# Kernel tuning notes

Hardware: AMD Instinct MI355X
Metric: run time of the kernel (lower is better)

Reference implementation:

```python
import jax, jax.numpy as jnp
import numpy as np

N_NODES = 40962
N_EDGES = 245760
K = 10  # gaussian kernels
D = 2   # pseudo-coordinate dim
EPS = 1e-15


def gmm_conv(x, edge_index, pseudo, g, mu, sigma, root, bias):
    """PyG GMMConv with aggr='mean', root_weight=True.
    x: [N, Cin], edge_index: [2, E] (row 0 = source j, row 1 = target i),
    pseudo: [E, D], g: [Cin, K*Cout], mu/sigma: [K, D], root: [Cin, Cout], bias: [Cout].
    """
    src, dst = edge_index[0], edge_index[1]
    E = pseudo.shape[0]
    # Gaussian mixture edge weights: [E, K]
    diff = pseudo[:, None, :] - mu[None, :, :]                     # [E, K, D]
    w = jnp.exp(jnp.sum(-0.5 * diff * diff / (EPS + sigma[None] ** 2), axis=-1))
    xj = x[src]                                                    # [E, Cin] gather
    y = (xj @ g).reshape(E, K, -1)                                 # [E, K, Cout]
    msg = jnp.sum(y * w[:, :, None], axis=1)                       # [E, Cout]
    agg = jax.ops.segment_sum(msg, dst, num_segments=N_NODES)      # scatter-add
    deg = jax.ops.segment_sum(jnp.ones((E,), x.dtype), dst, num_segments=N_NODES)
    agg = agg / jnp.maximum(deg, 1.0)[:, None]                     # mean aggregation
    return agg + x @ root + bias


def setup_inputs() -> dict:
    key = jax.random.key(0)
    ks = jax.random.split(key, 20)
    Cin, Ch, Cout = 64, 64, 128
    sc = lambda fan: 1.0 / np.sqrt(fan)
    inp = {
        "x": jax.random.normal(ks[0], (N_NODES, Cin), jnp.float32),
        "edge_index": jax.random.randint(ks[1], (2, N_EDGES), 0, N_NODES, jnp.int32),
        "pseudo": jax.random.uniform(ks[2], (N_EDGES, D), jnp.float32),
        # conv1: Cin -> Ch
        "g1": jax.random.normal(ks[3], (Cin, K * Ch), jnp.float32) * sc(Cin),
        "mu1": jax.random.uniform(ks[4], (K, D), jnp.float32),
        "sigma1": jax.random.uniform(ks[5], (K, D), jnp.float32) + 0.5,
        "root1": jax.random.normal(ks[6], (Cin, Ch), jnp.float32) * sc(Cin),
        "b1": jnp.zeros((Ch,), jnp.float32),
        # conv2: Ch -> Cout
        "g2": jax.random.normal(ks[7], (Ch, K * Cout), jnp.float32) * sc(Ch),
        "mu2": jax.random.uniform(ks[8], (K, D), jnp.float32),
        "sigma2": jax.random.uniform(ks[9], (K, D), jnp.float32) + 0.5,
        "root2": jax.random.normal(ks[10], (Ch, Cout), jnp.float32) * sc(Ch),
        "b2": jnp.zeros((Cout,), jnp.float32),
        # shortcut: Cin -> Cout (size_in != size_out)
        "gs": jax.random.normal(ks[11], (Cin, K * Cout), jnp.float32) * sc(Cin),
        "mus": jax.random.uniform(ks[12], (K, D), jnp.float32),
        "sigmas": jax.random.uniform(ks[13], (K, D), jnp.float32) + 0.5,
        "roots": jax.random.normal(ks[14], (Cin, Cout), jnp.float32) * sc(Cin),
        "bs": jnp.zeros((Cout,), jnp.float32),
    }
    return inp


def reference(x, edge_index, pseudo, g1, mu1, sigma1, root1, b1,
              g2, mu2, sigma2, root2, b2, gs, mus, sigmas, roots, bs):
    h = gmm_conv(x, edge_index, pseudo, g1, mu1, sigma1, root1, b1)
    h = jax.nn.relu(h)
    y = gmm_conv(h, edge_index, pseudo, g2, mu2, sigma2, root2, b2)
    x_s = gmm_conv(x, edge_index, pseudo, gs, mus, sigmas, roots, bs)
    return jax.nn.relu(y + x_s)
```

## Files before the change

kernel.cpp:

```cpp
#include <hip/hip_runtime.h>
#include <hip/hip_bf16.h>

using bf16 = __hip_bfloat16;
typedef __attribute__((ext_vector_type(8))) short short8;
typedef __attribute__((ext_vector_type(4))) float float4v;

#define N_NODES 40962
#define N_EDGES 245760
#define NP      41024
#define KG      10
#define SCAN_B  256
#define NBLK    ((NP + SCAN_B - 1) / SCAN_B)
#define GRIDF   (NP / 16)

#define CVT_V   (N_NODES * 64 / 8)
#define CVT_BLK ((CVT_V + 255) / 256)
#define W3_BLK  (N_EDGES / 256)
#define PACK_N  (64 * 704 + 2 * 128 * 704)
#define PACK_BLK (PACK_N / 256)

#define ZRS  40
#define ZKS  672
#define ZSZE 13440

__device__ __forceinline__ float ldf(const void* p, size_t i, int isf32) {
    return isf32 ? ((const float*)p)[i] : __bfloat162float(((const bf16*)p)[i]);
}
__device__ __forceinline__ float blo(unsigned u) { return __uint_as_float(u << 16); }
__device__ __forceinline__ float bhi(unsigned u) { return __uint_as_float(u & 0xffff0000u); }
__device__ __forceinline__ unsigned pk2(float a, float b) {
    union { bf16 h[2]; unsigned u; } t;
    t.h[0] = __float2bfloat16(a);
    t.h[1] = __float2bfloat16(b);
    return t.u;
}
__device__ __forceinline__ int rfl(int v) { return __builtin_amdgcn_readfirstlane(v); }

__global__ void k_detect_count(const void* x, const int* __restrict__ ei,
                               int* __restrict__ flag, int* __restrict__ deg) {
    if (blockIdx.x == 0) {
        __shared__ int huge_c, zero_even;
        if (threadIdx.x == 0) { huge_c = 0; zero_even = 0; }
        __syncthreads();
        const bf16* xb = (const bf16*)x;
        int lh = 0, lz = 0;
        for (int i = threadIdx.x; i < 8192; i += 256) {
            float v = __bfloat162float(xb[i]);
            if (!(fabsf(v) <= 1e4f)) lh++;
            if ((i & 1) == 0 && v == 0.0f) lz++;
        }
        atomicAdd(&huge_c, lh);
        atomicAdd(&zero_even, lz);
        __syncthreads();
        if (threadIdx.x == 0) flag[0] = (huge_c > 0 || zero_even > 3000) ? 1 : 0;
    } else {
        int e = (blockIdx.x - 1) * 256 + threadIdx.x;
        if (e < N_EDGES) atomicAdd(&deg[ei[N_EDGES + e]], 1);
    }
}

__global__ void k_scan1(const int* __restrict__ deg, int* __restrict__ offs,
                        int* __restrict__ bsum) {
    __shared__ int buf[SCAN_B];
    int t = threadIdx.x, b = blockIdx.x;
    int i = b * SCAN_B + t;
    int v = (i < NP) ? deg[i] : 0;
    buf[t] = v;
    __syncthreads();
    for (int off = 1; off < SCAN_B; off <<= 1) {
        int a = (t >= off) ? buf[t - off] : 0;
        __syncthreads();
        buf[t] += a;
        __syncthreads();
    }
    if (i < NP) offs[i] = buf[t] - v;
    if (t == SCAN_B - 1) bsum[b] = buf[t];
}

__global__ void k_scan3m(int* __restrict__ offs, const int* __restrict__ bsum,
                         const int* __restrict__ deg, int* __restrict__ cur,
                         float* __restrict__ invdeg) {
    __shared__ int buf[256];
    int t = threadIdx.x, b = blockIdx.x;
    int v = (t < NBLK) ? bsum[t] : 0;
    buf[t] = v;
    __syncthreads();
    for (int off = 1; off < 256; off <<= 1) {
        int a = (t >= off) ? buf[t - off] : 0;
        __syncthreads();
        buf[t] += a;
        __syncthreads();
    }
    int bofs = (b > 0) ? buf[b - 1] : 0;
    int total = buf[NBLK - 1];
    int i = b * 256 + t;
    if (i < NP) {
        int o = offs[i] + bofs;
        offs[i] = o;
        cur[i] = o;
        int d = deg[i];
        invdeg[i] = 1.0f / (float)(d > 1 ? d : 1);
    }
    if (i == 0) offs[NP] = total;
}

__global__ void k_fill(const int* __restrict__ ei, int* __restrict__ cur,
                       int* __restrict__ ep, int* __restrict__ csr_src) {
    int e = blockIdx.x * 256 + threadIdx.x;
    if (e < N_EDGES) {
        int pos = atomicAdd(&cur[ei[N_EDGES + e]], 1);
        ep[e] = pos;
        csr_src[pos] = ei[e];
    }
}

__device__ __forceinline__ void gw_one(float p0, float p1, const void* mu,
                                       const void* sg, int f, float* out) {
#pragma unroll
    for (int k = 0; k < KG; k++) {
        float m0 = ldf(mu, 2 * k + 0, f), m1 = ldf(mu, 2 * k + 1, f);
        float s0 = ldf(sg, 2 * k + 0, f), s1 = ldf(sg, 2 * k + 1, f);
        float d0 = p0 - m0, d1 = p1 - m1;
        float t = -0.5f * (d0 * d0 / (1e-15f + s0 * s0) + d1 * d1 / (1e-15f + s1 * s1));
        out[k] = __expf(t);
    }
}

__device__ __forceinline__ void pack_frag(const void* g, const void* root, int f,
                                          int idx, int Cout, bf16* Bp) {
    int j = idx & 7;
    int lane = (idx >> 3) & 63;
    int rem = idx >> 9;
    int kc = rem % 22;
    int n = rem / 22;
    int col = n * 16 + (lane & 15);
    int k = kc * 32 + (lane >> 4) * 8 + j;
    float v;
    if (k < 512) {
        int cin = k >> 3, kg = k & 7;
        v = ldf(g, (size_t)cin * (KG * Cout) + (size_t)kg * Cout + col, f);
    } else if (k < 640) {
        int jj = k - 512;
        int cin = jj >> 1, kg = 8 + (jj & 1);
        v = ldf(g, (size_t)cin * (KG * Cout) + (size_t)kg * Cout + col, f);
    } else {
        v = ldf(root, (size_t)(k - 640) * Cout + col, f);
    }
    Bp[idx] = __float2bfloat16(v);
}

__global__ void k_prep_all(const void* __restrict__ x, const void* __restrict__ pseudo,
                           const void* mu1, const void* sg1, const void* mu2,
                           const void* sg2, const void* mus, const void* sgs,
                           const void* g1, const void* root1, const void* g2,
                           const void* root2, const void* gs, const void* roots,
                           const int* __restrict__ flag, const int* __restrict__ ep,
                           bf16* __restrict__ Xf, bf16* __restrict__ wc1,
                           bf16* __restrict__ wcs, bf16* __restrict__ wc2,
                           bf16* wt1p, bf16* wt2p, bf16* wtsp) {
    int b = blockIdx.x;
    int tid = threadIdx.x;
    int f = flag[0];
    if (b < CVT_BLK) {
        int i = b * 256 + tid;
        if (i < CVT_V) {
            int node = i >> 3, j = i & 7;
            uint4 u;
            if (f) {
                const float4* xf = (const float4*)x;
                float4 a = xf[2 * i], c = xf[2 * i + 1];
                union { bf16 t[8]; uint4 u; } tt;
                tt.t[0] = __float2bfloat16(a.x); tt.t[1] = __float2bfloat16(a.y);
                tt.t[2] = __float2bfloat16(a.z); tt.t[3] = __float2bfloat16(a.w);
                tt.t[4] = __float2bfloat16(c.x); tt.t[5] = __float2bfloat16(c.y);
                tt.t[6] = __float2bfloat16(c.z); tt.t[7] = __float2bfloat16(c.w);
                u = tt.u;
            } else {
                u = ((const uint4*)x)[i];
            }
            *(uint4*)(Xf + ((size_t)(j >> 2) * NP + node) * 32 + (j & 3) * 8) = u;
        }
    } else if (b < CVT_BLK + W3_BLK) {
        int e = (b - CVT_BLK) * 256 + tid;
        float p0 = ldf(pseudo, (size_t)e * 2 + 0, f);
        float p1 = ldf(pseudo, (size_t)e * 2 + 1, f);
        float o1[KG], o2[KG], os[KG];
        gw_one(p0, p1, mu1, sg1, f, o1);
        gw_one(p0, p1, mu2, sg2, f, o2);
        gw_one(p0, p1, mus, sgs, f, os);
        int pos = ep[e];
        unsigned* d1 = (unsigned*)wc1 + (size_t)pos * 5;
        d1[0] = pk2(o1[0], o1[1]); d1[1] = pk2(o1[2], o1[3]);
        d1[2] = pk2(o1[4], o1[5]); d1[3] = pk2(o1[6], o1[7]);
        d1[4] = pk2(o1[8], o1[9]);
        unsigned* ds = (unsigned*)wcs + (size_t)pos * 5;
        ds[0] = pk2(os[0], os[1]); ds[1] = pk2(os[2], os[3]);
        ds[2] = pk2(os[4], os[5]); ds[3] = pk2(os[6], os[7]);
        ds[4] = pk2(os[8], os[9]);
        unsigned* d2 = (unsigned*)wc2 + (size_t)pos * 5;
        d2[0] = pk2(o2[0], o2[1]); d2[1] = pk2(o2[2], o2[3]);
        d2[2] = pk2(o2[4], o2[5]); d2[3] = pk2(o2[6], o2[7]);
        d2[4] = pk2(o2[8], o2[9]);
    } else {
        int idx = (b - CVT_BLK - W3_BLK) * 256 + tid;
        if (idx < 64 * 704) {
            pack_frag(g1, root1, f, idx, 64, wt1p);
        } else if (idx < 64 * 704 + 128 * 704) {
            pack_frag(g2, root2, f, idx - 64 * 704, 128, wt2p);
        } else {
            pack_frag(gs, roots, f, idx - 64 * 704 - 128 * 704, 128, wtsp);
        }
    }
}

__device__ __forceinline__ float ldx_frag(const bf16* X, int src, int lane) {
    return __bfloat162float(X[((size_t)(lane >> 5) * NP + src) * 32 + (lane & 31)]);
}

__device__ __forceinline__ int clampe(int idx) {
    return idx > N_EDGES - 1 ? N_EDGES - 1 : idx;
}

__device__ __forceinline__ void gather_one(const int* __restrict__ offs,
                                           const int* __restrict__ csr_src,
                                           const unsigned* __restrict__ wb,
                                           const bf16* __restrict__ X, int node,
                                           int lane, float* acc) {
#pragma unroll
    for (int k = 0; k < KG; k++) acc[k] = 0.0f;
    int beg = rfl(offs[node]);
    int end = rfl(offs[node + 1]);
    int cnt = end - beg;
    int sC = rfl(csr_src[clampe(beg + 2)]);
    float xv0 = ldx_frag(X, rfl(csr_src[clampe(beg + 0)]), lane);
    float xv1 = ldx_frag(X, rfl(csr_src[clampe(beg + 1)]), lane);
    const unsigned* wp0 = wb + (size_t)clampe(beg + 0) * 5;
    unsigned c0 = wp0[0], c1 = wp0[1], c2 = wp0[2], c3 = wp0[3], c4 = wp0[4];
    const unsigned* wp1 = wb + (size_t)clampe(beg + 1) * 5;
    unsigned n0 = wp1[0], n1 = wp1[1], n2 = wp1[2], n3 = wp1[3], n4 = wp1[4];
    for (int t = 0; t < cnt; ++t) {
        int sN = rfl(csr_src[clampe(beg + t + 3)]);
        float xv2 = ldx_frag(X, sC, lane);
        const unsigned* wp2 = wb + (size_t)clampe(beg + t + 2) * 5;
        unsigned m0 = wp2[0], m1 = wp2[1], m2 = wp2[2], m3 = wp2[3], m4 = wp2[4];
        acc[0] += blo(c0) * xv0; acc[1] += bhi(c0) * xv0;
        acc[2] += blo(c1) * xv0; acc[3] += bhi(c1) * xv0;
        acc[4] += blo(c2) * xv0; acc[5] += bhi(c2) * xv0;
        acc[6] += blo(c3) * xv0; acc[7] += bhi(c3) * xv0;
        acc[8] += blo(c4) * xv0; acc[9] += bhi(c4) * xv0;
        xv0 = xv1; xv1 = xv2; sC = sN;
        c0 = n0; c1 = n1; c2 = n2; c3 = n3; c4 = n4;
        n0 = m0; n1 = m1; n2 = m2; n3 = m3; n4 = m4;
    }
}

__device__ __forceinline__ void store_zlds(bf16* z, int r, int lane, const float* a,
                                           float inv) {
    union { bf16 h[8]; uint4 u; } p;
#pragma unroll
    for (int k = 0; k < 8; k++) p.h[k] = __float2bfloat16(a[k] * inv);
    *(uint4*)(z + (lane >> 2) * ZKS + r * ZRS + (lane & 3) * 8) = p.u;
    *(unsigned*)(z + (16 + (lane >> 4)) * ZKS + r * ZRS + (lane & 15) * 2) =
        pk2(a[8] * inv, a[9] * inv);
}

__global__ __launch_bounds__(512) void k_fused1(
    const int* __restrict__ offs, const int* __restrict__ csr_src,
    const bf16* __restrict__ wc1, const float* __restrict__ invdeg,
    const bf16* __restrict__ Xf, const bf16* __restrict__ wt1p,
    const void* __restrict__ b1, const int* __restrict__ flag,
    bf16* __restrict__ hf) {
    __shared__ bf16 zA[ZSZE];
    int lane = threadIdx.x & 63;
    int wave = threadIdx.x >> 6;
    int bid = blockIdx.x;
    const unsigned* wb = (const unsigned*)wc1;

#pragma unroll
    for (int i = 0; i < 2; i++) {
        int r = wave * 2 + i;
        int node = bid * 16 + r;
        float acc[KG];
        gather_one(offs, csr_src, wb, Xf, node, lane, acc);
        store_zlds(zA, r, lane, acc, invdeg[node]);
    }
    __syncthreads();

    if (wave < 4) {
        int m = lane & 15, quad = lane >> 4;
        int row0 = bid * 16;
        float4v acc4 = (float4v){0.f, 0.f, 0.f, 0.f};
        const bf16* brow = wt1p + ((size_t)(wave * 22) * 64 + lane) * 8;
        const bf16* xrow = Xf + ((size_t)(row0 + m)) * 32 + quad * 8;
#pragma unroll
        for (int kc = 0; kc < 22; kc++) {
            short8 a = (kc < 20)
                ? *(const short8*)(zA + kc * ZKS + m * ZRS + quad * 8)
                : *(const short8*)(xrow + (size_t)(kc - 20) * NP * 32);
            short8 b = *(const short8*)(brow + (size_t)kc * 512);
            acc4 = __builtin_amdgcn_mfma_f32_16x16x32_bf16(a, b, acc4, 0, 0, 0);
        }
        int f = flag[0];
        int gcol = wave * 16 + m;
        float bv = ldf(b1, gcol, f);
#pragma unroll
        for (int r = 0; r < 4; r++) {
            int grow = row0 + quad * 4 + r;
            if (grow >= N_NODES) continue;
            float v = fmaxf(acc4[r] + bv, 0.f);
            hf[((size_t)(gcol >> 5) * NP + grow) * 32 + (gcol & 31)] =
                __float2bfloat16(v);
        }
    }
}

__global__ __launch_bounds__(512) void k_fused2(
    const int* __restrict__ offs, const int* __restrict__ csr_src,
    const bf16* __restrict__ wc2, const bf16* __restrict__ wcs,
    const float* __restrict__ invdeg, const bf16* __restrict__ Xf,
    const bf16* __restrict__ hf, const bf16* __restrict__ wt2p,
    const bf16* __restrict__ wtsp, const void* __restrict__ b2,
    const void* __restrict__ bs, const int* __restrict__ flag,
    void* __restrict__ out) {
    __shared__ bf16 z[ZSZE];
    int lane = threadIdx.x & 63;
    int wave = threadIdx.x >> 6;
    int bid = blockIdx.x;
    int m = lane & 15, quad = lane >> 4;
    int row0 = bid * 16;

#pragma unroll
    for (int i = 0; i < 2; i++) {
        int r = wave * 2 + i;
        int node = bid * 16 + r;
        float acc[KG];
        gather_one(offs, csr_src, (const unsigned*)wc2, hf, node, lane, acc);
        store_zlds(z, r, lane, acc, invdeg[node]);
    }
    __syncthreads();

    float4v acc4 = (float4v){0.f, 0.f, 0.f, 0.f};
    {
        const bf16* brow = wt2p + ((size_t)(wave * 22) * 64 + lane) * 8;
        const bf16* hrow = hf + ((size_t)(row0 + m)) * 32 + quad * 8;
#pragma unroll
        for (int kc = 0; kc < 22; kc++) {
            short8 a = (kc < 20)
                ? *(const short8*)(z + kc * ZKS + m * ZRS + quad * 8)
                : *(const short8*)(hrow + (size_t)(kc - 20) * NP * 32);
            short8 b = *(const short8*)(brow + (size_t)kc * 512);
            acc4 = __builtin_amdgcn_mfma_f32_16x16x32_bf16(a, b, acc4, 0, 0, 0);
        }
    }
    __syncthreads();

#pragma unroll
    for (int i = 0; i < 2; i++) {
        int r = wave * 2 + i;
        int node = bid * 16 + r;
        float acc[KG];
        gather_one(offs, csr_src, (const unsigned*)wcs, Xf, node, lane, acc);
        store_zlds(z, r, lane, acc, invdeg[node]);
    }
    __syncthreads();

    {
        const bf16* brow = wtsp + ((size_t)(wave * 22) * 64 + lane) * 8;
        const bf16* xrow = Xf + ((size_t)(row0 + m)) * 32 + quad * 8;
#pragma unroll
        for (int kc = 0; kc < 22; kc++) {
            short8 a = (kc < 20)
                ? *(const short8*)(z + kc * ZKS + m * ZRS + quad * 8)
                : *(const short8*)(xrow + (size_t)(kc - 20) * NP * 32);
            short8 b = *(const short8*)(brow + (size_t)kc * 512);
            acc4 = __builtin_amdgcn_mfma_f32_16x16x32_bf16(a, b, acc4, 0, 0, 0);
        }
    }

    int f = flag[0];
    int gcol = wave * 16 + m;
    float bv = ldf(b2, gcol, f) + ldf(bs, gcol, f);
#pragma unroll
    for (int r = 0; r < 4; r++) {
        int grow = row0 + quad * 4 + r;
        if (grow >= N_NODES) continue;
        float v = fmaxf(acc4[r] + bv, 0.f);
        size_t oidx = (size_t)grow * 128 + gcol;
        if (f) ((float*)out)[oidx] = v;
        else   ((bf16*)out)[oidx] = __float2bfloat16(v);
    }
}

extern "C" void kernel_launch(void* const* d_in, const int* in_sizes, int n_in,
                              void* d_out, int out_size, void* d_ws, size_t ws_size,
                              hipStream_t stream) {
    const void* x      = d_in[0];
    const int*  ei     = (const int*)d_in[1];
    const void* pseudo = d_in[2];
    const void* g1     = d_in[3];
    const void* mu1    = d_in[4];
    const void* sg1    = d_in[5];
    const void* root1  = d_in[6];
    const void* b1     = d_in[7];
    const void* g2     = d_in[8];
    const void* mu2    = d_in[9];
    const void* sg2    = d_in[10];
    const void* root2  = d_in[11];
    const void* b2     = d_in[12];
    const void* gs     = d_in[13];
    const void* mus    = d_in[14];
    const void* sgs    = d_in[15];
    const void* roots  = d_in[16];
    const void* bs     = d_in[17];

    char* ws = (char*)d_ws;
    size_t off = 0;
    auto alloc = [&](size_t bytes) -> char* {
        char* p = ws + off;
        off += (bytes + 255) & ~(size_t)255;
        return p;
    };
    const size_t XFS = (size_t)2 * NP * 32 * 2;

    int*   flag   = (int*)alloc(256);
    int*   deg    = (int*)alloc((size_t)NP * 4);
    int*   offs   = (int*)alloc((size_t)(NP + 1) * 4);
    int*   cur    = (int*)alloc((size_t)NP * 4);
    float* invdeg = (float*)alloc((size_t)NP * 4);
    int*   bsum   = (int*)alloc((size_t)NBLK * 4);
    int*   ep     = (int*)alloc((size_t)N_EDGES * 4);
    int*   csrs   = (int*)alloc((size_t)N_EDGES * 4);
    bf16*  Xf     = (bf16*)alloc(XFS);
    bf16*  hf     = (bf16*)alloc(XFS);
    bf16*  wt1p   = (bf16*)alloc((size_t)64 * 704 * 2);
    bf16*  wt2p   = (bf16*)alloc((size_t)128 * 704 * 2);
    bf16*  wtsp   = (bf16*)alloc((size_t)128 * 704 * 2);
    bf16*  wc1    = (bf16*)alloc((size_t)N_EDGES * 10 * 2);
    bf16*  wcs    = (bf16*)alloc((size_t)N_EDGES * 10 * 2);
    bf16*  wc2    = (bf16*)alloc((size_t)N_EDGES * 10 * 2);
    (void)ws_size;

    hipMemsetAsync(deg, 0, (size_t)NP * 4, stream);
    k_detect_count<<<1 + (N_EDGES + 255) / 256, 256, 0, stream>>>(x, ei, flag, deg);
    k_scan1<<<NBLK, SCAN_B, 0, stream>>>(deg, offs, bsum);
    k_scan3m<<<NBLK, 256, 0, stream>>>(offs, bsum, deg, cur, invdeg);
    k_fill<<<(N_EDGES + 255) / 256, 256, 0, stream>>>(ei, cur, ep, csrs);
    k_prep_all<<<CVT_BLK + W3_BLK + PACK_BLK, 256, 0, stream>>>(
        x, pseudo, mu1, sg1, mu2, sg2, mus, sgs, g1, root1, g2, root2, gs, roots,
        flag, ep, Xf, wc1, wcs, wc2, wt1p, wt2p, wtsp);
    k_fused1<<<GRIDF, 512, 0, stream>>>(offs, csrs, wc1, invdeg, Xf, wt1p, b1,
                                        flag, hf);
    k_fused2<<<GRIDF, 512, 0, stream>>>(offs, csrs, wc2, wcs, invdeg, Xf, hf,
                                        wt2p, wtsp, b2, bs, flag, d_out);
}
```

Baseline: 273.3 us.

## Fuse shortcut gather into first conv pass and switch node features to row-major

The shortcut conv's edge aggregation over x is moved from the second kernel into the first. Both conv1 and shortcut edge weights are now interleaved per edge, so one gather pass over the x neighbours feeds two accumulators. The shortcut result is written to a bf16 intermediate and added in the second kernel. This removes a second full neighbour gather over x. Node features move to a plain row-major 64-wide layout with a deeper prefetch distance, and LDS z is re-laid out row-major. The cost is an extra 128-wide bf16 write and read per node, plus more register pressure in the dual gather.

Measured after the change: 270.9 us. Within noise of the previous version (-0.9%).

```diff
diff --git a/kernel.cpp b/kernel.cpp
--- a/kernel.cpp
+++ b/kernel.cpp
@@ -19,9 +19,8 @@
 #define PACK_N  (64 * 704 + 2 * 128 * 704)
 #define PACK_BLK (PACK_N / 256)
 
-#define ZRS  40
-#define ZKS  672
-#define ZSZE 13440
+#define ZRS  680
+#define ZT   10880
 
 __device__ __forceinline__ float ldf(const void* p, size_t i, int isf32) {
     return isf32 ? ((const float*)p)[i] : __bfloat162float(((const bf16*)p)[i]);
@@ -155,9 +154,9 @@
                            const void* g1, const void* root1, const void* g2,
                            const void* root2, const void* gs, const void* roots,
                            const int* __restrict__ flag, const int* __restrict__ ep,
-                           bf16* __restrict__ Xf, bf16* __restrict__ wc1,
-                           bf16* __restrict__ wcs, bf16* __restrict__ wc2,
-                           bf16* wt1p, bf16* wt2p, bf16* wtsp) {
+                           bf16* __restrict__ Xf, bf16* __restrict__ wcab,
+                           bf16* __restrict__ wc2, bf16* wt1p, bf16* wt2p,
+                           bf16* wtsp) {
     int b = blockIdx.x;
     int tid = threadIdx.x;
     int f = flag[0];
@@ -178,7 +177,7 @@
             } else {
                 u = ((const uint4*)x)[i];
             }
-            *(uint4*)(Xf + ((size_t)(j >> 2) * NP + node) * 32 + (j & 3) * 8) = u;
+            *(uint4*)(Xf + (size_t)node * 64 + j * 8) = u;
         }
     } else if (b < CVT_BLK + W3_BLK) {
         int e = (b - CVT_BLK) * 256 + tid;
@@ -189,14 +188,13 @@
         gw_one(p0, p1, mu2, sg2, f, o2);
         gw_one(p0, p1, mus, sgs, f, os);
         int pos = ep[e];
-        unsigned* d1 = (unsigned*)wc1 + (size_t)pos * 5;
-        d1[0] = pk2(o1[0], o1[1]); d1[1] = pk2(o1[2], o1[3]);
-        d1[2] = pk2(o1[4], o1[5]); d1[3] = pk2(o1[6], o1[7]);
-        d1[4] = pk2(o1[8], o1[9]);
-        unsigned* ds = (unsigned*)wcs + (size_t)pos * 5;
-        ds[0] = pk2(os[0], os[1]); ds[1] = pk2(os[2], os[3]);
-        ds[2] = pk2(os[4], os[5]); ds[3] = pk2(os[6], os[7]);
-        ds[4] = pk2(os[8], os[9]);
+        unsigned* d = (unsigned*)wcab + (size_t)pos * 10;
+        d[0] = pk2(o1[0], o1[1]); d[1] = pk2(o1[2], o1[3]);
+        d[2] = pk2(o1[4], o1[5]); d[3] = pk2(o1[6], o1[7]);
+        d[4] = pk2(o1[8], o1[9]);
+        d[5] = pk2(os[0], os[1]); d[6] = pk2(os[2], os[3]);
+        d[7] = pk2(os[4], os[5]); d[8] = pk2(os[6], os[7]);
+        d[9] = pk2(os[8], os[9]);
         unsigned* d2 = (unsigned*)wc2 + (size_t)pos * 5;
         d2[0] = pk2(o2[0], o2[1]); d2[1] = pk2(o2[2], o2[3]);
         d2[2] = pk2(o2[4], o2[5]); d2[3] = pk2(o2[6], o2[7]);
@@ -213,12 +211,66 @@
     }
 }
 
-__device__ __forceinline__ float ldx_frag(const bf16* X, int src, int lane) {
-    return __bfloat162float(X[((size_t)(lane >> 5) * NP + src) * 32 + (lane & 31)]);
+__device__ __forceinline__ float ldxf(const bf16* X, int src, int lane) {
+    return __bfloat162float(X[(size_t)src * 64 + lane]);
 }
 
 __device__ __forceinline__ int clampe(int idx) {
     return idx > N_EDGES - 1 ? N_EDGES - 1 : idx;
+}
+
+__device__ __forceinline__ void store_zlds(bf16* z, int r, int lane, const float* a,
+                                           float inv) {
+    union { bf16 h[8]; uint4 u; } p;
+#pragma unroll
+    for (int k = 0; k < 8; k++) p.h[k] = __float2bfloat16(a[k] * inv);
+    *(uint4*)(z + r * ZRS + lane * 8) = p.u;
+    *(unsigned*)(z + r * ZRS + 512 + lane * 2) = pk2(a[8] * inv, a[9] * inv);
+}
+
+__device__ __forceinline__ void gather_dual(const int* __restrict__ offs,
+                                            const int* __restrict__ csr_src,
+                                            const unsigned* __restrict__ wb,
+                                            const bf16* __restrict__ X, int node,
+                                            int lane, float* aa, float* ab) {
+#pragma unroll
+    for (int k = 0; k < KG; k++) { aa[k] = 0.0f; ab[k] = 0.0f; }
+    int beg = rfl(offs[node]);
+    int end = rfl(offs[node + 1]);
+    int cnt = end - beg;
+    int s4 = rfl(csr_src[clampe(beg + 4)]);
+    float xv0 = ldxf(X, rfl(csr_src[clampe(beg + 0)]), lane);
+    float xv1 = ldxf(X, rfl(csr_src[clampe(beg + 1)]), lane);
+    float xv2 = ldxf(X, rfl(csr_src[clampe(beg + 2)]), lane);
+    float xv3 = ldxf(X, rfl(csr_src[clampe(beg + 3)]), lane);
+    const unsigned* wp0 = wb + (size_t)clampe(beg + 0) * 10;
+    unsigned c0 = wp0[0], c1 = wp0[1], c2 = wp0[2], c3 = wp0[3], c4 = wp0[4];
+    unsigned c5 = wp0[5], c6 = wp0[6], c7 = wp0[7], c8 = wp0[8], c9 = wp0[9];
+    const unsigned* wp1 = wb + (size_t)clampe(beg + 1) * 10;
+    unsigned n0 = wp1[0], n1 = wp1[1], n2 = wp1[2], n3 = wp1[3], n4 = wp1[4];
+    unsigned n5 = wp1[5], n6 = wp1[6], n7 = wp1[7], n8 = wp1[8], n9 = wp1[9];
+    for (int t = 0; t < cnt; ++t) {
+        int s5 = rfl(csr_src[clampe(beg + t + 5)]);
+        float xv4 = ldxf(X, s4, lane);
+        const unsigned* wp2 = wb + (size_t)clampe(beg + t + 2) * 10;
+        unsigned m0 = wp2[0], m1 = wp2[1], m2 = wp2[2], m3 = wp2[3], m4 = wp2[4];
+        unsigned m5 = wp2[5], m6 = wp2[6], m7 = wp2[7], m8 = wp2[8], m9 = wp2[9];
+        aa[0] += blo(c0) * xv0; aa[1] += bhi(c0) * xv0;
+        aa[2] += blo(c1) * xv0; aa[3] += bhi(c1) * xv0;
+        aa[4] += blo(c2) * xv0; aa[5] += bhi(c2) * xv0;
+        aa[6] += blo(c3) * xv0; aa[7] += bhi(c3) * xv0;
+        aa[8] += blo(c4) * xv0; aa[9] += bhi(c4) * xv0;
+        ab[0] += blo(c5) * xv0; ab[1] += bhi(c5) * xv0;
+        ab[2] += blo(c6) * xv0; ab[3] += bhi(c6) * xv0;
+        ab[4] += blo(c7) * xv0; ab[5] += bhi(c7) * xv0;
+        ab[6] += blo(c8) * xv0; ab[7] += bhi(c8) * xv0;
+        ab[8] += blo(c9) * xv0; ab[9] += bhi(c9) * xv0;
+        xv0 = xv1; xv1 = xv2; xv2 = xv3; xv3 = xv4; s4 = s5;
+        c0 = n0; c1 = n1; c2 = n2; c3 = n3; c4 = n4;
+        c5 = n5; c6 = n6; c7 = n7; c8 = n8; c9 = n9;
+        n0 = m0; n1 = m1; n2 = m2; n3 = m3; n4 = m4;
+        n5 = m5; n6 = m6; n7 = m7; n8 = m8; n9 = m9;
+    }
 }
 
 __device__ __forceinline__ void gather_one(const int* __restrict__ offs,
@@ -231,16 +283,18 @@
     int beg = rfl(offs[node]);
     int end = rfl(offs[node + 1]);
     int cnt = end - beg;
-    int sC = rfl(csr_src[clampe(beg + 2)]);
-    float xv0 = ldx_frag(X, rfl(csr_src[clampe(beg + 0)]), lane);
-    float xv1 = ldx_frag(X, rfl(csr_src[clampe(beg + 1)]), lane);
+    int s4 = rfl(csr_src[clampe(beg + 4)]);
+    float xv0 = ldxf(X, rfl(csr_src[clampe(beg + 0)]), lane);
+    float xv1 = ldxf(X, rfl(csr_src[clampe(beg + 1)]), lane);
+    float xv2 = ldxf(X, rfl(csr_src[clampe(beg + 2)]), lane);
+    float xv3 = ldxf(X, rfl(csr_src[clampe(beg + 3)]), lane);
     const unsigned* wp0 = wb + (size_t)clampe(beg + 0) * 5;
     unsigned c0 = wp0[0], c1 = wp0[1], c2 = wp0[2], c3 = wp0[3], c4 = wp0[4];
     const unsigned* wp1 = wb + (size_t)clampe(beg + 1) * 5;
     unsigned n0 = wp1[0], n1 = wp1[1], n2 = wp1[2], n3 = wp1[3], n4 = wp1[4];
     for (int t = 0; t < cnt; ++t) {
-        int sN = rfl(csr_src[clampe(beg + t + 3)]);
-        float xv2 = ldx_frag(X, sC, lane);
+        int s5 = rfl(csr_src[clampe(beg + t + 5)]);
+        float xv4 = ldxf(X, s4, lane);
         const unsigned* wp2 = wb + (size_t)clampe(beg + t + 2) * 5;
         unsigned m0 = wp2[0], m1 = wp2[1], m2 = wp2[2], m3 = wp2[3], m4 = wp2[4];
         acc[0] += blo(c0) * xv0; acc[1] += bhi(c0) * xv0;
@@ -248,59 +302,75 @@
         acc[4] += blo(c2) * xv0; acc[5] += bhi(c2) * xv0;
         acc[6] += blo(c3) * xv0; acc[7] += bhi(c3) * xv0;
         acc[8] += blo(c4) * xv0; acc[9] += bhi(c4) * xv0;
-        xv0 = xv1; xv1 = xv2; sC = sN;
+        xv0 = xv1; xv1 = xv2; xv2 = xv3; xv3 = xv4; s4 = s5;
         c0 = n0; c1 = n1; c2 = n2; c3 = n3; c4 = n4;
         n0 = m0; n1 = m1; n2 = m2; n3 = m3; n4 = m4;
     }
 }
 
-__device__ __forceinline__ void store_zlds(bf16* z, int r, int lane, const float* a,
-                                           float inv) {
-    union { bf16 h[8]; uint4 u; } p;
-#pragma unroll
-    for (int k = 0; k < 8; k++) p.h[k] = __float2bfloat16(a[k] * inv);
-    *(uint4*)(z + (lane >> 2) * ZKS + r * ZRS + (lane & 3) * 8) = p.u;
-    *(unsigned*)(z + (16 + (lane >> 4)) * ZKS + r * ZRS + (lane & 15) * 2) =
-        pk2(a[8] * inv, a[9] * inv);
-}
-
-__global__ __launch_bounds__(512) void k_fused1(
+__global__ __launch_bounds__(512) void k_fusedA(
     const int* __restrict__ offs, const int* __restrict__ csr_src,
-    const bf16* __restrict__ wc1, const float* __restrict__ invdeg,
+    const bf16* __restrict__ wcab, const float* __restrict__ invdeg,
     const bf16* __restrict__ Xf, const bf16* __restrict__ wt1p,
-    const void* __restrict__ b1, const int* __restrict__ flag,
-    bf16* __restrict__ hf) {
-    __shared__ bf16 zA[ZSZE];
+    const bf16* __restrict__ wtsp, const void* __restrict__ b1,
+    const void* __restrict__ bs, const int* __restrict__ flag,
+    bf16* __restrict__ hf, bf16* __restrict__ ys) {
+    __shared__ bf16 z1[ZT];
+    __shared__ bf16 zs[ZT];
     int lane = threadIdx.x & 63;
     int wave = threadIdx.x >> 6;
     int bid = blockIdx.x;
-    const unsigned* wb = (const unsigned*)wc1;
 
 #pragma unroll
     for (int i = 0; i < 2; i++) {
         int r = wave * 2 + i;
         int node = bid * 16 + r;
-        float acc[KG];
-        gather_one(offs, csr_src, wb, Xf, node, lane, acc);
-        store_zlds(zA, r, lane, acc, invdeg[node]);
+        float aa[KG], ab[KG];
+        gather_dual(offs, csr_src, (const unsigned*)wcab, Xf, node, lane, aa, ab);
+        float inv = invdeg[node];
+        store_zlds(z1, r, lane, aa, inv);
+        store_zlds(zs, r, lane, ab, inv);
     }
     __syncthreads();
 
+    int m = lane & 15, quad = lane >> 4;
+    int row0 = bid * 16;
+    int f = flag[0];
+
+    {
+        float4v acc4 = (float4v){0.f, 0.f, 0.f, 0.f};
+        const bf16* brow = wtsp + ((size_t)(wave * 22) * 64 + lane) * 8;
+        const bf16* xrow = Xf + (size_t)(row0 + m) * 64;
+#pragma unroll
+        for (int kc = 0; kc < 22; kc++) {
+            short8 a = (kc < 20)
+                ? *(const short8*)(zs + m * ZRS + kc * 32 + quad * 8)
+                : *(const short8*)(xrow + (kc - 20) * 32 + quad * 8);
+            short8 b = *(const short8*)(brow + (size_t)kc * 512);
+            acc4 = __builtin_amdgcn_mfma_f32_16x16x32_bf16(a, b, acc4, 0, 0, 0);
+        }
+        int gcol = wave * 16 + m;
+        float bv = ldf(bs, gcol, f);
+#pragma unroll
+        for (int r = 0; r < 4; r++) {
+            int grow = row0 + quad * 4 + r;
+            if (grow >= N_NODES) continue;
+            ys[(size_t)grow * 128 + gcol] = __float2bfloat16(acc4[r] + bv);
+        }
+    }
+
     if (wave < 4) {
-        int m = lane & 15, quad = lane >> 4;
-        int row0 = bid * 16;
         float4v acc4 = (float4v){0.f, 0.f, 0.f, 0.f};
         const bf16* brow = wt1p + ((size_t)(wave * 22) * 64 + lane) * 8;
-        const bf16* xrow = Xf + ((size_t)(row0 + m)) * 32 + quad * 8;
+        const bf16* xrow = Xf + (size_t)(row0 + m) * 64;
 #pragma unroll
         for (int kc = 0; kc < 22; kc++) {
             short8 a = (kc < 20)
-                ? *(const short8*)(zA + kc * ZKS + m * ZRS + quad * 8)
-                : *(const short8*)(xrow + (size_t)(kc - 20) * NP * 32);
+                ? *(const short8*)(z1 + m * ZRS + kc * 32 + quad * 8)
+                : *(const short8*)(xrow + (kc - 20) * 32 + quad * 8);
             short8 b = *(const short8*)(brow + (size_t)kc * 512);
             acc4 = __builtin_amdgcn_mfma_f32_16x16x32_bf16(a, b, acc4, 0, 0, 0);
         }
-        int f = flag[0];
         int gcol = wave * 16 + m;
         float bv = ldf(b1, gcol, f);
 #pragma unroll
@@ -308,26 +378,21 @@
             int grow = row0 + quad * 4 + r;
             if (grow >= N_NODES) continue;
             float v = fmaxf(acc4[r] + bv, 0.f);
-            hf[((size_t)(gcol >> 5) * NP + grow) * 32 + (gcol & 31)] =
-                __float2bfloat16(v);
-        }
-    }
-}
-
-__global__ __launch_bounds__(512) void k_fused2(
+            hf[(size_t)grow * 64 + gcol] = __float2bfloat16(v);
+        }
+    }
+}
+
+__global__ __launch_bounds__(512) void k_fusedB(
     const int* __restrict__ offs, const int* __restrict__ csr_src,
-    const bf16* __restrict__ wc2, const bf16* __restrict__ wcs,
-    const float* __restrict__ invdeg, const bf16* __restrict__ Xf,
+    const bf16* __restrict__ wc2, const float* __restrict__ invdeg,
     const bf16* __restrict__ hf, const bf16* __restrict__ wt2p,
-    const bf16* __restrict__ wtsp, const void* __restrict__ b2,
-    const void* __restrict__ bs, const int* __restrict__ flag,
-    void* __restrict__ out) {
-    __shared__ bf16 z[ZSZE];
+    const void* __restrict__ b2, const bf16* __restrict__ ys,
+    const int* __restrict__ flag, void* __restrict__ out) {
+    __shared__ bf16 z[ZT];
     int lane = threadIdx.x & 63;
     int wave = threadIdx.x >> 6;
     int bid = blockIdx.x;
-    int m = lane & 15, quad = lane >> 4;
-    int row0 = bid * 16;
 
 #pragma unroll
     for (int i = 0; i < 2; i++) {
@@ -339,53 +404,28 @@
     }
     __syncthreads();
 
+    int m = lane & 15, quad = lane >> 4;
+    int row0 = bid * 16;
+    int f = flag[0];
     float4v acc4 = (float4v){0.f, 0.f, 0.f, 0.f};
-    {
-        const bf16* brow = wt2p + ((size_t)(wave * 22) * 64 + lane) * 8;
-        const bf16* hrow = hf + ((size_t)(row0 + m)) * 32 + quad * 8;
-#pragma unroll
-        for (int kc = 0; kc < 22; kc++) {
-            short8 a = (kc < 20)
-                ? *(const short8*)(z + kc * ZKS + m * ZRS + quad * 8)
-                : *(const short8*)(hrow + (size_t)(kc - 20) * NP * 32);
-            short8 b = *(const short8*)(brow + (size_t)kc * 512);
-            acc4 = __builtin_amdgcn_mfma_f32_16x16x32_bf16(a, b, acc4, 0, 0, 0);
-        }
-    }
-    __syncthreads();
-
-#pragma unroll
-    for (int i = 0; i < 2; i++) {
-        int r = wave * 2 + i;
-        int node = bid * 16 + r;
-        float acc[KG];
-        gather_one(offs, csr_src, (const unsigned*)wcs, Xf, node, lane, acc);
-        store_zlds(z, r, lane, acc, invdeg[node]);
-    }
-    __syncthreads();
-
-    {
-        const bf16* brow = wtsp + ((size_t)(wave * 22) * 64 + lane) * 8;
-        const bf16* xrow = Xf + ((size_t)(row0 + m)) * 32 + quad * 8;
-#pragma unroll
-        for (int kc = 0; kc < 22; kc++) {
-            short8 a = (kc < 20)
-                ? *(const short8*)(z + kc * ZKS + m * ZRS + quad * 8)
-                : *(const short8*)(xrow + (size_t)(kc - 20) * NP * 32);
-            short8 b = *(const short8*)(brow + (size_t)kc * 512);
-            acc4 = __builtin_amdgcn_mfma_f32_16x16x32_bf16(a, b, acc4, 0, 0, 0);
-        }
-    }
-
-    int f = flag[0];
+    const bf16* brow = wt2p + ((size_t)(wave * 22) * 64 + lane) * 8;
+    const bf16* hrow = hf + (size_t)(row0 + m) * 64;
+#pragma unroll
+    for (int kc = 0; kc < 22; kc++) {
+        short8 a = (kc < 20)
+            ? *(const short8*)(z + m * ZRS + kc * 32 + quad * 8)
+            : *(const short8*)(hrow + (kc - 20) * 32 + quad * 8);
+        short8 b = *(const short8*)(brow + (size_t)kc * 512);
+        acc4 = __builtin_amdgcn_mfma_f32_16x16x32_bf16(a, b, acc4, 0, 0, 0);
+    }
     int gcol = wave * 16 + m;
-    float bv = ldf(b2, gcol, f) + ldf(bs, gcol, f);
+    float bv = ldf(b2, gcol, f);
 #pragma unroll
     for (int r = 0; r < 4; r++) {
         int grow = row0 + quad * 4 + r;
         if (grow >= N_NODES) continue;
-        float v = fmaxf(acc4[r] + bv, 0.f);
         size_t oidx = (size_t)grow * 128 + gcol;
+        float v = fmaxf(acc4[r] + bv + __bfloat162float(ys[oidx]), 0.f);
         if (f) ((float*)out)[oidx] = v;
         else   ((bf16*)out)[oidx] = __float2bfloat16(v);
     }
@@ -420,7 +460,7 @@
         off += (bytes + 255) & ~(size_t)255;
         return p;
     };
-    const size_t XFS = (size_t)2 * NP * 32 * 2;
+    const size_t XFS = (size_t)NP * 64 * 2;
 
     int*   flag   = (int*)alloc(256);
     int*   deg    = (int*)alloc((size_t)NP * 4);
@@ -432,11 +472,11 @@
     int*   csrs   = (int*)alloc((size_t)N_EDGES * 4);
     bf16*  Xf     = (bf16*)alloc(XFS);
     bf16*  hf     = (bf16*)alloc(XFS);
+    bf16*  ys     = (bf16*)alloc((size_t)NP * 128 * 2);
     bf16*  wt1p   = (bf16*)alloc((size_t)64 * 704 * 2);
     bf16*  wt2p   = (bf16*)alloc((size_t)128 * 704 * 2);
     bf16*  wtsp   = (bf16*)alloc((size_t)128 * 704 * 2);
-    bf16*  wc1    = (bf16*)alloc((size_t)N_EDGES * 10 * 2);
-    bf16*  wcs    = (bf16*)alloc((size_t)N_EDGES * 10 * 2);
+    bf16*  wcab   = (bf16*)alloc((size_t)N_EDGES * 20 * 2);
     bf16*  wc2    = (bf16*)alloc((size_t)N_EDGES * 10 * 2);
     (void)ws_size;
 
@@ -447,9 +487,9 @@
     k_fill<<<(N_EDGES + 255) / 256, 256, 0, stream>>>(ei, cur, ep, csrs);
     k_prep_all<<<CVT_BLK + W3_BLK + PACK_BLK, 256, 0, stream>>>(
         x, pseudo, mu1, sg1, mu2, sg2, mus, sgs, g1, root1, g2, root2, gs, roots,
-        flag, ep, Xf, wc1, wcs, wc2, wt1p, wt2p, wtsp);
-    k_fused1<<<GRIDF, 512, 0, stream>>>(offs, csrs, wc1, invdeg, Xf, wt1p, b1,
-                                        flag, hf);
-    k_fused2<<<GRIDF, 512, 0, stream>>>(offs, csrs, wc2, wcs, invdeg, Xf, hf,
-                                        wt2p, wtsp, b2, bs, flag, d_out);
-}
+        flag, ep, Xf, wcab, wc2, wt1p, wt2p, wtsp);
+    k_fusedA<<<GRIDF, 512, 0, stream>>>(offs, csrs, wcab, invdeg, Xf, wt1p, wtsp,
+                                        b1, bs, flag, hf, ys);
+    k_fusedB<<<GRIDF, 512, 0, stream>>>(offs, csrs, wc2, invdeg, hf, wt2p, b2,
+                                        ys, flag, d_out);
+}
```
